# Kernel optimization log

Hardware: AMD Instinct MI355X
Metric: run time of the kernel (lower is better)

Reference implementation:

```python
import jax, jax.numpy as jnp
import numpy as np

V, E, H, L, B, T = 32000, 1024, 1024, 2, 64, 512


def setup_inputs() -> dict:
    key = jax.random.key(0)
    ks = jax.random.split(key, 20)
    s = 0.02  # init scale for params
    n = jax.random.normal
    return {
        "input_tokens": jax.random.randint(ks[0], (1, B), 0, V),
        "h0": n(ks[1], (L, B, H), jnp.float32),
        "c0": n(ks[2], (L, B, H), jnp.float32),
        "encoder_outputs": n(ks[3], (T, B, H), jnp.float32),
        "emb_table": n(ks[4], (V, E), jnp.float32) * s,
        "attn_W": n(ks[5], (H, 2 * H), jnp.float32) * s,
        "attn_b": jnp.zeros((H,), jnp.float32),
        "attn_v": n(ks[6], (H,), jnp.float32) * s,
        "w_ih0": n(ks[7], (4 * H, 2 * E), jnp.float32) * s,
        "w_hh0": n(ks[8], (4 * H, H), jnp.float32) * s,
        "b_ih0": jnp.zeros((4 * H,), jnp.float32),
        "b_hh0": jnp.zeros((4 * H,), jnp.float32),
        "w_ih1": n(ks[9], (4 * H, H), jnp.float32) * s,
        "w_hh1": n(ks[10], (4 * H, H), jnp.float32) * s,
        "b_ih1": jnp.zeros((4 * H,), jnp.float32),
        "b_hh1": jnp.zeros((4 * H,), jnp.float32),
        "out_W": n(ks[11], (V, H), jnp.float32) * s,
        "out_b": jnp.zeros((V,), jnp.float32),
    }


def lstm_cell(x, h, c, w_ih, w_hh, b_ih, b_hh):
    # torch LSTM gate order: i, f, g, o
    g = x @ w_ih.T + h @ w_hh.T + b_ih + b_hh
    i, f, gg, o = jnp.split(g, 4, axis=-1)
    c2 = jax.nn.sigmoid(f) * c + jax.nn.sigmoid(i) * jnp.tanh(gg)
    h2 = jax.nn.sigmoid(o) * jnp.tanh(c2)
    return h2, c2


def reference(input_tokens, h0, c0, encoder_outputs, emb_table, attn_W, attn_b,
              attn_v, w_ih0, w_hh0, b_ih0, b_hh0, w_ih1, w_hh1, b_ih1, b_hh1,
              out_W, out_b):
    emb = emb_table[input_tokens]            # [1, B, E]
    h_top = h0[-1]                           # [B, H]
    # concat attention: score[b,t] = v . (attn_W @ [h_b ; e_tb] + attn_b)
    cat = jnp.concatenate(
        [jnp.broadcast_to(h_top[None], encoder_outputs.shape), encoder_outputs],
        axis=-1)                              # [T, B, 2H]
    scores = jnp.einsum('tbk,hk,h->bt', cat, attn_W, attn_v) \
        + jnp.dot(attn_b, attn_v)            # [B, T]
    attn = jax.nn.softmax(scores, axis=1)    # [B, T]
    context = jnp.einsum('bt,tbh->bh', attn, encoder_outputs)  # [B, H]
    x = jnp.concatenate([context, emb[0]], axis=-1)            # [B, 2E]
    h1, c1 = lstm_cell(x, h0[0], c0[0], w_ih0, w_hh0, b_ih0, b_hh0)
    h2, c2 = lstm_cell(h1, h0[1], c0[1], w_ih1, w_hh1, b_ih1, b_hh1)
    logits = h2 @ out_W.T + out_b            # [B, V]
    out = jax.nn.log_softmax(logits, axis=1)
    h_n = jnp.stack([h1, h2])
    c_n = jnp.stack([c1, c2])
    return out, h_n, c_n, attn[:, None, :]
```

## Files before the change

kernel.cpp:

```cpp
#include <hip/hip_runtime.h>

#define V 32000
#define B 64
#define T 512
#define H 1024

typedef short bf16x8 __attribute__((ext_vector_type(8)));
typedef float f32x4 __attribute__((ext_vector_type(4)));

__device__ inline unsigned short f2bf(float x) {
    unsigned int u = __float_as_uint(x);
    return (unsigned short)((u + 0x7FFFu + ((u >> 16) & 1u)) >> 16);
}

__global__ void prep_misc(const int* __restrict__ tok, const float* __restrict__ emb,
                          const float* __restrict__ h0, unsigned short* __restrict__ xcat0,
                          unsigned short* __restrict__ xcat1, const float4* __restrict__ W4,
                          const float* __restrict__ v, float4* __restrict__ u2p) {
    int blk = blockIdx.x;
    int tid = threadIdx.x;
    if (blk < 256) {
        int idx = blk * 256 + tid;
        int b = idx >> 10, e = idx & 1023;
        xcat0[(size_t)b * 3072 + 1024 + e] = f2bf(emb[(size_t)tok[b] * 1024 + e]);
    } else if (blk < 768) {
        int idx = (blk - 256) * 256 + tid;
        int layer = idx >> 16;
        int r = idx & 65535;
        int b = r >> 10, k = r & 1023;
        float vv = h0[layer * 65536 + b * 1024 + k];
        if (layer == 0) xcat0[(size_t)b * 3072 + 2048 + k] = f2bf(vv);
        else            xcat1[(size_t)b * 2048 + 1024 + k] = f2bf(vv);
    } else {
        int hc = blk - 768;
        float4 acc = {0.f, 0.f, 0.f, 0.f};
#pragma unroll 4
        for (int i = 0; i < 32; ++i) {
            int h = hc * 32 + i;
            float vv = v[h];
            float4 w = W4[(size_t)h * 512 + 256 + tid];
            acc.x += vv * w.x; acc.y += vv * w.y; acc.z += vv * w.z; acc.w += vv * w.w;
        }
        u2p[hc * 256 + tid] = acc;
    }
}

__global__ void u2_reduce(const float4* __restrict__ u2p, float4* __restrict__ u2) {
    int k4 = threadIdx.x;
    float4 acc = {0.f, 0.f, 0.f, 0.f};
#pragma unroll
    for (int hc = 0; hc < 32; ++hc) {
        float4 p = u2p[hc * 256 + k4];
        acc.x += p.x; acc.y += p.y; acc.z += p.z; acc.w += p.w;
    }
    u2[k4] = acc;
}

__global__ __launch_bounds__(256) void attn_fused(
    const float4* __restrict__ enc4, const float4* __restrict__ u2,
    float* __restrict__ scores, float2* __restrict__ pms, float4* __restrict__ ctxp) {
    int b = blockIdx.x;
    int tc = blockIdx.y;
    int tid = threadIdx.x;
    int wid = tid >> 6, lane = tid & 63;
    float4 u[4];
#pragma unroll
    for (int i = 0; i < 4; ++i) u[i] = u2[lane + 64 * i];
    float m = -1e30f, s = 0.f;
    float4 acc[4] = {{0,0,0,0},{0,0,0,0},{0,0,0,0},{0,0,0,0}};
    int t0 = tc * 32 + wid * 8;
    for (int tt = 0; tt < 8; ++tt) {
        int t = t0 + tt;
        const float4* e = enc4 + ((size_t)t * B + b) * 256;
        float4 e4[4];
#pragma unroll
        for (int i = 0; i < 4; ++i) e4[i] = e[lane + 64 * i];
        float d = 0.f;
#pragma unroll
        for (int i = 0; i < 4; ++i)
            d += e4[i].x * u[i].x + e4[i].y * u[i].y + e4[i].z * u[i].z + e4[i].w * u[i].w;
#pragma unroll
        for (int off = 32; off; off >>= 1) d += __shfl_xor(d, off);
        if (lane == 0) scores[b * T + t] = d;
        float mn = fmaxf(m, d);
        float sc = expf(m - mn);
        float w = expf(d - mn);
        s = s * sc + w;
#pragma unroll
        for (int i = 0; i < 4; ++i) {
            acc[i].x = acc[i].x * sc + w * e4[i].x;
            acc[i].y = acc[i].y * sc + w * e4[i].y;
            acc[i].z = acc[i].z * sc + w * e4[i].z;
            acc[i].w = acc[i].w * sc + w * e4[i].w;
        }
        m = mn;
    }
    __shared__ float4 lacc[4][256];
    __shared__ float lm[4], ls[4];
#pragma unroll
    for (int i = 0; i < 4; ++i) lacc[wid][lane + 64 * i] = acc[i];
    if (lane == 0) { lm[wid] = m; ls[wid] = s; }
    __syncthreads();
    float M = fmaxf(fmaxf(lm[0], lm[1]), fmaxf(lm[2], lm[3]));
    float e0 = expf(lm[0] - M), e1 = expf(lm[1] - M);
    float e2 = expf(lm[2] - M), e3 = expf(lm[3] - M);
    float S = ls[0] * e0 + ls[1] * e1 + ls[2] * e2 + ls[3] * e3;
    float4 c0 = lacc[0][tid], c1 = lacc[1][tid], c2 = lacc[2][tid], c3 = lacc[3][tid];
    float4 c;
    c.x = c0.x * e0 + c1.x * e1 + c2.x * e2 + c3.x * e3;
    c.y = c0.y * e0 + c1.y * e1 + c2.y * e2 + c3.y * e3;
    c.z = c0.z * e0 + c1.z * e1 + c2.z * e2 + c3.z * e3;
    c.w = c0.w * e0 + c1.w * e1 + c2.w * e2 + c3.w * e3;
    ctxp[((size_t)tc * B + b) * 256 + tid] = c;
    if (tid == 0) pms[tc * B + b] = make_float2(M, S);
}

__global__ void attn_combine(const float4* __restrict__ ctxp, const float2* __restrict__ pms,
                             const float* __restrict__ scores, unsigned short* __restrict__ xcat0,
                             float* __restrict__ attn_out) {
    int b = blockIdx.x, tid = threadIdx.x;
    float M = -1e30f, S = 0.f;
#pragma unroll
    for (int tc = 0; tc < 16; ++tc) {
        float2 p = pms[tc * B + b];
        float mn = fmaxf(M, p.x);
        S = S * expf(M - mn) + p.y * expf(p.x - mn);
        M = mn;
    }
    float inv = 1.f / S;
    float4 c = {0.f, 0.f, 0.f, 0.f};
#pragma unroll
    for (int tc = 0; tc < 16; ++tc) {
        float w = expf(pms[tc * B + b].x - M);
        float4 v = ctxp[((size_t)tc * B + b) * 256 + tid];
        c.x += w * v.x; c.y += w * v.y; c.z += w * v.z; c.w += w * v.w;
    }
    c.x *= inv; c.y *= inv; c.z *= inv; c.w *= inv;
    unsigned short* d = xcat0 + (size_t)b * 3072 + tid * 4;
    d[0] = f2bf(c.x); d[1] = f2bf(c.y); d[2] = f2bf(c.z); d[3] = f2bf(c.w);
#pragma unroll
    for (int j = 0; j < 2; ++j) {
        int t = j * 256 + tid;
        attn_out[b * T + t] = expf(scores[b * T + t] - M) * inv;
    }
}

struct MJob {
    const float* W1; int ldw1;
    const float* W2; int ldw2;
    int seg;
    const unsigned short* A; int lda;
    float* out; int ldo; long outz;
    const float* bias;
    int kblk;
};

template <int NT>
__global__ __launch_bounds__(256) void mfma_gemm(MJob job) {
    constexpr int CHB = NT * 512;
    __shared__ __align__(16) char Wlds[2 * CHB];
    int tid = threadIdx.x;
    int l = tid & 63;
    int mt = __builtin_amdgcn_readfirstlane(tid >> 6);
    int l15 = l & 15, l4 = l >> 4;
    int n0 = blockIdx.x * NT;
    int kbase = blockIdx.z * job.kblk;
    float* outp = job.out + (size_t)blockIdx.z * job.outz;
    f32x4 acc[NT / 16];
#pragma unroll
    for (int i = 0; i < NT / 16; ++i) acc[i] = (f32x4){0.f, 0.f, 0.f, 0.f};
    int nch = job.kblk >> 7;

    auto stageW = [&](int kg, int bi) {
        const float* Wb; int ldw, koff;
        if (kg < job.seg) { Wb = job.W1; ldw = job.ldw1; koff = kg; }
        else              { Wb = job.W2; ldw = job.ldw2; koff = kg - job.seg; }
        char* base = &Wlds[bi * CHB];
#pragma unroll
        for (int i = 0; i < NT / 8; ++i) {
            int gl = i * 256 + tid;
            int row = gl >> 5, gp = gl & 31;
            int G = gp ^ (row & 7);
            const float* src = Wb + (size_t)(n0 + row) * ldw + koff + G * 4;
            char* dst = base + (i * 4096 + (tid & 192) * 16);
            __builtin_amdgcn_global_load_lds(
                (const __attribute__((address_space(1))) void*)src,
                (__attribute__((address_space(3))) void*)dst, 16, 0, 0);
        }
    };

    stageW(kbase, 0);
    __syncthreads();
    int cur = 0;
    for (int c = 0; c < nch; ++c) {
        int kg = kbase + c * 128;
        bf16x8 af[4];
        const unsigned short* arow = job.A + (size_t)(mt * 16 + l15) * job.lda + kg + l4 * 8;
#pragma unroll
        for (int s = 0; s < 4; ++s) af[s] = *(const bf16x8*)(arow + s * 32);
        if (c + 1 < nch) stageW(kbase + (c + 1) * 128, cur ^ 1);
        const char* rb = &Wlds[cur * CHB];
#pragma unroll
        for (int jt = 0; jt < NT / 16; ++jt) {
            int row = jt * 16 + l15;
            const char* rbase = rb + row * 512;
            int x = row & 7;
#pragma unroll
            for (int s = 0; s < 4; ++s) {
                int G0 = 2 * l4 + 8 * s;
                uint4 wa = *(const uint4*)(rbase + ((G0 ^ x) << 4));
                uint4 wb = *(const uint4*)(rbase + (((G0 + 1) ^ x) << 4));
                union { bf16x8 f; unsigned int u[4]; } bu;
                bu.u[0] = __builtin_amdgcn_perm(wa.y, wa.x, 0x07060302u);
                bu.u[1] = __builtin_amdgcn_perm(wa.w, wa.z, 0x07060302u);
                bu.u[2] = __builtin_amdgcn_perm(wb.y, wb.x, 0x07060302u);
                bu.u[3] = __builtin_amdgcn_perm(wb.w, wb.z, 0x07060302u);
                acc[jt] = __builtin_amdgcn_mfma_f32_16x16x32_bf16(af[s], bu.f, acc[jt], 0, 0, 0);
            }
        }
        __syncthreads();
        cur ^= 1;
    }
#pragma unroll
    for (int jt = 0; jt < NT / 16; ++jt) {
        int n = n0 + jt * 16 + l15;
        float bv = job.bias ? job.bias[n] : 0.f;
#pragma unroll
        for (int r = 0; r < 4; ++r) {
            int m = mt * 16 + l4 * 4 + r;
            outp[(size_t)m * job.ldo + n] = acc[jt][r] + bv;
        }
    }
}

__global__ void lstm_elem(const float* __restrict__ gp, int gz,
                          const float* __restrict__ b_ih, const float* __restrict__ b_hh,
                          const float* __restrict__ c_prev, float* __restrict__ h_out,
                          float* __restrict__ c_out, unsigned short* __restrict__ hbf,
                          int hbf_ld) {
    int idx = blockIdx.x * 256 + threadIdx.x;
    int b = idx >> 10, k = idx & 1023;
    float g[4];
#pragma unroll
    for (int gt = 0; gt < 4; ++gt) {
        float s = b_ih[gt * 1024 + k] + b_hh[gt * 1024 + k];
        for (int z = 0; z < gz; ++z)
            s += gp[(size_t)z * 262144 + (size_t)b * 4096 + gt * 1024 + k];
        g[gt] = s;
    }
    float i_ = 1.f / (1.f + expf(-g[0]));
    float f_ = 1.f / (1.f + expf(-g[1]));
    float gg = tanhf(g[2]);
    float o_ = 1.f / (1.f + expf(-g[3]));
    float c = f_ * c_prev[b * 1024 + k] + i_ * gg;
    float h = o_ * tanhf(c);
    c_out[b * 1024 + k] = c;
    h_out[b * 1024 + k] = h;
    hbf[(size_t)b * hbf_ld + k] = f2bf(h);
}

__global__ void lse_partial(const float4* __restrict__ logits4, float* __restrict__ pm,
                            float* __restrict__ ps) {
    int bi = blockIdx.x;
    int b = bi >> 4, c = bi & 15;
    int tid = threadIdx.x;
    const float4* row = logits4 + (size_t)b * 8000 + c * 500;
    float m = -1e30f, s = 0.f;
#pragma unroll
    for (int i = 0; i < 2; ++i) {
        int v = i * 256 + tid;
        if (v < 500) {
            float4 x = row[v];
            float m1 = fmaxf(fmaxf(x.x, x.y), fmaxf(x.z, x.w));
            if (m1 > m) { s = s * expf(m - m1); m = m1; }
            s += expf(x.x - m) + expf(x.y - m) + expf(x.z - m) + expf(x.w - m);
        }
    }
#pragma unroll
    for (int off = 32; off; off >>= 1) {
        float m2 = __shfl_xor(m, off);
        float s2 = __shfl_xor(s, off);
        float mn = fmaxf(m, m2);
        s = s * expf(m - mn) + s2 * expf(m2 - mn);
        m = mn;
    }
    __shared__ float mred[4], sred[4];
    int wid = tid >> 6, lane = tid & 63;
    if (lane == 0) { mred[wid] = m; sred[wid] = s; }
    __syncthreads();
    if (tid == 0) {
        float M = mred[0], S = sred[0];
        for (int i = 1; i < 4; ++i) {
            float mn = fmaxf(M, mred[i]);
            S = S * expf(M - mn) + sred[i] * expf(mred[i] - mn);
            M = mn;
        }
        pm[bi] = M;
        ps[bi] = S;
    }
}

__global__ void lse_sub(float4* __restrict__ logits4, const float* __restrict__ pm,
                        const float* __restrict__ ps) {
    int b = blockIdx.y;
    float M = pm[b * 16], S = ps[b * 16];
#pragma unroll
    for (int i = 1; i < 16; ++i) {
        float m2 = pm[b * 16 + i];
        float mn = fmaxf(M, m2);
        S = S * expf(M - mn) + ps[b * 16 + i] * expf(m2 - mn);
        M = mn;
    }
    float l = M + logf(S);
    int v4 = blockIdx.x * 256 + threadIdx.x;
    if (v4 < 8000) {
        float4 x = logits4[(size_t)b * 8000 + v4];
        x.x -= l; x.y -= l; x.z -= l; x.w -= l;
        logits4[(size_t)b * 8000 + v4] = x;
    }
}

extern "C" void kernel_launch(void* const* d_in, const int* in_sizes, int n_in,
                              void* d_out, int out_size, void* d_ws, size_t ws_size,
                              hipStream_t stream) {
    const int*   tok   = (const int*)d_in[0];
    const float* h0    = (const float*)d_in[1];
    const float* c0    = (const float*)d_in[2];
    const float* enc   = (const float*)d_in[3];
    const float* emb   = (const float*)d_in[4];
    const float* attnW = (const float*)d_in[5];
    const float* attnv = (const float*)d_in[7];
    const float* w_ih0 = (const float*)d_in[8];
    const float* w_hh0 = (const float*)d_in[9];
    const float* b_ih0 = (const float*)d_in[10];
    const float* b_hh0 = (const float*)d_in[11];
    const float* w_ih1 = (const float*)d_in[12];
    const float* w_hh1 = (const float*)d_in[13];
    const float* b_ih1 = (const float*)d_in[14];
    const float* b_hh1 = (const float*)d_in[15];
    const float* out_W = (const float*)d_in[16];
    const float* out_b = (const float*)d_in[17];
    float* out = (float*)d_out;
    float* ws = (float*)d_ws;

    float* u2     = ws;
    float* u2p    = ws + 1024;
    float* scores = ws + 33792;
    float2* pms   = (float2*)(ws + 66560);
    unsigned short* xcat0 = (unsigned short*)(ws + 68608);
    unsigned short* xcat1 = (unsigned short*)(ws + 166912);
    unsigned short* h2bf  = (unsigned short*)(ws + 232448);
    float* pm     = ws + 265216;
    float* ps     = ws + 266240;

    float* out_logits = out;
    float* out_h1 = out + 2048000;
    float* out_h2 = out + 2113536;
    float* out_c1 = out + 2179072;
    float* out_c2 = out + 2244608;
    float* out_attn = out + 2310144;

    float* ctxp  = out;
    float* gpart = out;

    prep_misc<<<800, 256, 0, stream>>>(tok, emb, h0, xcat0, xcat1,
                                       (const float4*)attnW, attnv, (float4*)u2p);
    u2_reduce<<<1, 256, 0, stream>>>((const float4*)u2p, (float4*)u2);
    attn_fused<<<dim3(64, 16), 256, 0, stream>>>((const float4*)enc, (const float4*)u2,
                                                 scores, pms, (float4*)ctxp);
    attn_combine<<<64, 256, 0, stream>>>((const float4*)ctxp, pms, scores, xcat0, out_attn);

    {
        MJob j = {w_ih0, 2048, w_hh0, 1024, 2048, xcat0, 3072,
                  gpart, 4096, 262144L, nullptr, 768};
        mfma_gemm<64><<<dim3(64, 1, 4), 256, 0, stream>>>(j);
    }
    lstm_elem<<<256, 256, 0, stream>>>(gpart, 4, b_ih0, b_hh0, c0,
                                       out_h1, out_c1, xcat1, 2048);

    {
        MJob j = {w_ih1, 1024, w_hh1, 1024, 1024, xcat1, 2048,
                  gpart, 4096, 262144L, nullptr, 512};
        mfma_gemm<64><<<dim3(64, 1, 4), 256, 0, stream>>>(j);
    }
    lstm_elem<<<256, 256, 0, stream>>>(gpart, 4, b_ih1, b_hh1, c0 + 65536,
                                       out_h2, out_c2, h2bf, 1024);

    {
        MJob j = {out_W, 1024, nullptr, 0, 1 << 30, h2bf, 1024,
                  out_logits, V, 0L, out_b, 1024};
        mfma_gemm<32><<<dim3(1000, 1, 1), 256, 0, stream>>>(j);
    }

    lse_partial<<<1024, 256, 0, stream>>>((const float4*)out_logits, pm, ps);
    lse_sub<<<dim3(32, 64), 256, 0, stream>>>((float4*)out_logits, pm, ps);
}
```

Baseline: 147.7 us.

## Overlap attention with context-independent LSTM gate GEMM slices in one fused launch

Merges the attention kernel with GEMM blocks that compute the layer-0 embedding/hidden K-slices and the layer-1 hidden-state slice, which do not depend on the attention context. These run concurrently in one launch, so the remaining post-attention GEMMs handle only one K-slice each. It also moves the partial buffers into separate workspace regions and branches the online softmax update to skip one exp. The cost is a heterogeneous kernel whose shared-memory size and register use are set by the larger path, plus more partial-sum traffic.

```diff
diff --git a/kernel.cpp b/kernel.cpp
--- a/kernel.cpp
+++ b/kernel.cpp
@@ -56,63 +56,160 @@
     u2[k4] = acc;
 }
 
-__global__ __launch_bounds__(256) void attn_fused(
+struct GSlice {
+    const float* W1; int ldw1;
+    const float* W2; int ldw2;
+    int seg;
+    const unsigned short* A; int lda;
+    float* out;
+    int kbase;
+};
+
+__global__ __launch_bounds__(256) void mega1(
     const float4* __restrict__ enc4, const float4* __restrict__ u2,
-    float* __restrict__ scores, float2* __restrict__ pms, float4* __restrict__ ctxp) {
-    int b = blockIdx.x;
-    int tc = blockIdx.y;
+    float* __restrict__ scores, float2* __restrict__ pms, float4* __restrict__ ctxp,
+    GSlice s0, GSlice s1, GSlice s2) {
+    __shared__ __align__(16) char smem[32768];
+    int bx = blockIdx.x;
     int tid = threadIdx.x;
     int wid = tid >> 6, lane = tid & 63;
-    float4 u[4];
-#pragma unroll
-    for (int i = 0; i < 4; ++i) u[i] = u2[lane + 64 * i];
-    float m = -1e30f, s = 0.f;
-    float4 acc[4] = {{0,0,0,0},{0,0,0,0},{0,0,0,0},{0,0,0,0}};
-    int t0 = tc * 32 + wid * 8;
-    for (int tt = 0; tt < 8; ++tt) {
-        int t = t0 + tt;
-        const float4* e = enc4 + ((size_t)t * B + b) * 256;
-        float4 e4[4];
-#pragma unroll
-        for (int i = 0; i < 4; ++i) e4[i] = e[lane + 64 * i];
-        float d = 0.f;
-#pragma unroll
-        for (int i = 0; i < 4; ++i)
-            d += e4[i].x * u[i].x + e4[i].y * u[i].y + e4[i].z * u[i].z + e4[i].w * u[i].w;
-#pragma unroll
-        for (int off = 32; off; off >>= 1) d += __shfl_xor(d, off);
-        if (lane == 0) scores[b * T + t] = d;
-        float mn = fmaxf(m, d);
-        float sc = expf(m - mn);
-        float w = expf(d - mn);
-        s = s * sc + w;
+
+    if (bx < 1024) {
+        int b = bx & 63, tc = bx >> 6;
+        float4* lacc = (float4*)smem;
+        float* lm = (float*)(smem + 16384);
+        float* ls = (float*)(smem + 16384 + 16);
+        float4 u[4];
+#pragma unroll
+        for (int i = 0; i < 4; ++i) u[i] = u2[lane + 64 * i];
+        float m = -1e30f, s = 0.f;
+        float4 acc[4] = {{0,0,0,0},{0,0,0,0},{0,0,0,0},{0,0,0,0}};
+        int t0 = tc * 32 + wid * 8;
+        for (int tt = 0; tt < 8; ++tt) {
+            int t = t0 + tt;
+            const float4* e = enc4 + ((size_t)t * B + b) * 256;
+            float4 e4[4];
+#pragma unroll
+            for (int i = 0; i < 4; ++i) e4[i] = e[lane + 64 * i];
+            float d = 0.f;
+#pragma unroll
+            for (int i = 0; i < 4; ++i)
+                d += e4[i].x * u[i].x + e4[i].y * u[i].y + e4[i].z * u[i].z + e4[i].w * u[i].w;
+#pragma unroll
+            for (int off = 32; off; off >>= 1) d += __shfl_xor(d, off);
+            if (lane == 0) scores[b * T + t] = d;
+            if (d > m) {
+                float sc = expf(m - d);
+                s = s * sc + 1.f;
+#pragma unroll
+                for (int i = 0; i < 4; ++i) {
+                    acc[i].x = acc[i].x * sc + e4[i].x;
+                    acc[i].y = acc[i].y * sc + e4[i].y;
+                    acc[i].z = acc[i].z * sc + e4[i].z;
+                    acc[i].w = acc[i].w * sc + e4[i].w;
+                }
+                m = d;
+            } else {
+                float w = expf(d - m);
+                s += w;
+#pragma unroll
+                for (int i = 0; i < 4; ++i) {
+                    acc[i].x += w * e4[i].x;
+                    acc[i].y += w * e4[i].y;
+                    acc[i].z += w * e4[i].z;
+                    acc[i].w += w * e4[i].w;
+                }
+            }
+        }
+#pragma unroll
+        for (int i = 0; i < 4; ++i) lacc[wid * 256 + lane + 64 * i] = acc[i];
+        if (lane == 0) { lm[wid] = m; ls[wid] = s; }
+        __syncthreads();
+        float M = fmaxf(fmaxf(lm[0], lm[1]), fmaxf(lm[2], lm[3]));
+        float e0 = expf(lm[0] - M), e1 = expf(lm[1] - M);
+        float e2 = expf(lm[2] - M), e3 = expf(lm[3] - M);
+        float S = ls[0] * e0 + ls[1] * e1 + ls[2] * e2 + ls[3] * e3;
+        float4 c0 = lacc[0 * 256 + tid], c1 = lacc[1 * 256 + tid];
+        float4 c2 = lacc[2 * 256 + tid], c3 = lacc[3 * 256 + tid];
+        float4 c;
+        c.x = c0.x * e0 + c1.x * e1 + c2.x * e2 + c3.x * e3;
+        c.y = c0.y * e0 + c1.y * e1 + c2.y * e2 + c3.y * e3;
+        c.z = c0.z * e0 + c1.z * e1 + c2.z * e2 + c3.z * e3;
+        c.w = c0.w * e0 + c1.w * e1 + c2.w * e2 + c3.w * e3;
+        ctxp[((size_t)tc * B + b) * 256 + tid] = c;
+        if (tid == 0) pms[tc * B + b] = make_float2(M, S);
+        return;
+    }
+
+    int idx = bx - 1024;
+    GSlice g = (idx < 128) ? s0 : (idx < 256) ? s1 : s2;
+    int nb = idx & 127;
+    int l15 = lane & 15, l4 = lane >> 4;
+    int mt = __builtin_amdgcn_readfirstlane(wid);
+    int n0 = nb * 32;
+    f32x4 acc[2];
+    acc[0] = (f32x4){0.f, 0.f, 0.f, 0.f};
+    acc[1] = (f32x4){0.f, 0.f, 0.f, 0.f};
+
+    auto stageW = [&](int kg, int bi) {
+        const float* Wb; int ldw, koff;
+        if (kg < g.seg) { Wb = g.W1; ldw = g.ldw1; koff = kg; }
+        else            { Wb = g.W2; ldw = g.ldw2; koff = kg - g.seg; }
+        char* base = &smem[bi * 16384];
 #pragma unroll
         for (int i = 0; i < 4; ++i) {
-            acc[i].x = acc[i].x * sc + w * e4[i].x;
-            acc[i].y = acc[i].y * sc + w * e4[i].y;
-            acc[i].z = acc[i].z * sc + w * e4[i].z;
-            acc[i].w = acc[i].w * sc + w * e4[i].w;
-        }
-        m = mn;
-    }
-    __shared__ float4 lacc[4][256];
-    __shared__ float lm[4], ls[4];
-#pragma unroll
-    for (int i = 0; i < 4; ++i) lacc[wid][lane + 64 * i] = acc[i];
-    if (lane == 0) { lm[wid] = m; ls[wid] = s; }
+            int gl = i * 256 + tid;
+            int row = gl >> 5, gp = gl & 31;
+            int G = gp ^ (row & 7);
+            const float* src = Wb + (size_t)(n0 + row) * ldw + koff + G * 4;
+            char* dst = base + (i * 4096 + (tid & 192) * 16);
+            __builtin_amdgcn_global_load_lds(
+                (const __attribute__((address_space(1))) void*)src,
+                (__attribute__((address_space(3))) void*)dst, 16, 0, 0);
+        }
+    };
+
+    stageW(g.kbase, 0);
     __syncthreads();
-    float M = fmaxf(fmaxf(lm[0], lm[1]), fmaxf(lm[2], lm[3]));
-    float e0 = expf(lm[0] - M), e1 = expf(lm[1] - M);
-    float e2 = expf(lm[2] - M), e3 = expf(lm[3] - M);
-    float S = ls[0] * e0 + ls[1] * e1 + ls[2] * e2 + ls[3] * e3;
-    float4 c0 = lacc[0][tid], c1 = lacc[1][tid], c2 = lacc[2][tid], c3 = lacc[3][tid];
-    float4 c;
-    c.x = c0.x * e0 + c1.x * e1 + c2.x * e2 + c3.x * e3;
-    c.y = c0.y * e0 + c1.y * e1 + c2.y * e2 + c3.y * e3;
-    c.z = c0.z * e0 + c1.z * e1 + c2.z * e2 + c3.z * e3;
-    c.w = c0.w * e0 + c1.w * e1 + c2.w * e2 + c3.w * e3;
-    ctxp[((size_t)tc * B + b) * 256 + tid] = c;
-    if (tid == 0) pms[tc * B + b] = make_float2(M, S);
+    int cur = 0;
+    for (int c = 0; c < 8; ++c) {
+        int kg = g.kbase + c * 128;
+        bf16x8 af[4];
+        const unsigned short* arow = g.A + (size_t)(mt * 16 + l15) * g.lda + kg + l4 * 8;
+#pragma unroll
+        for (int s = 0; s < 4; ++s) af[s] = *(const bf16x8*)(arow + s * 32);
+        if (c + 1 < 8) stageW(g.kbase + (c + 1) * 128, cur ^ 1);
+        const char* rb = &smem[cur * 16384];
+#pragma unroll
+        for (int jt = 0; jt < 2; ++jt) {
+            int row = jt * 16 + l15;
+            const char* rbase = rb + row * 512;
+            int x = row & 7;
+#pragma unroll
+            for (int s = 0; s < 4; ++s) {
+                int G0 = 2 * l4 + 8 * s;
+                uint4 wa = *(const uint4*)(rbase + ((G0 ^ x) << 4));
+                uint4 wb = *(const uint4*)(rbase + (((G0 + 1) ^ x) << 4));
+                union { bf16x8 f; unsigned int u[4]; } bu;
+                bu.u[0] = __builtin_amdgcn_perm(wa.y, wa.x, 0x07060302u);
+                bu.u[1] = __builtin_amdgcn_perm(wa.w, wa.z, 0x07060302u);
+                bu.u[2] = __builtin_amdgcn_perm(wb.y, wb.x, 0x07060302u);
+                bu.u[3] = __builtin_amdgcn_perm(wb.w, wb.z, 0x07060302u);
+                acc[jt] = __builtin_amdgcn_mfma_f32_16x16x32_bf16(af[s], bu.f, acc[jt], 0, 0, 0);
+            }
+        }
+        __syncthreads();
+        cur ^= 1;
+    }
+#pragma unroll
+    for (int jt = 0; jt < 2; ++jt) {
+        int n = n0 + jt * 16 + l15;
+#pragma unroll
+        for (int r = 0; r < 4; ++r) {
+            int m2 = mt * 16 + l4 * 4 + r;
+            g.out[(size_t)m2 * 4096 + n] = acc[jt][r];
+        }
+    }
 }
 
 __global__ void attn_combine(const float4* __restrict__ ctxp, const float2* __restrict__ pms,
@@ -352,6 +449,9 @@
     unsigned short* h2bf  = (unsigned short*)(ws + 232448);
     float* pm     = ws + 265216;
     float* ps     = ws + 266240;
+    float* ctxp   = ws + 524288;
+    float* gpartL0 = ws + 1572864;
+    float* gpartL1 = ws + 2359296;
 
     float* out_logits = out;
     float* out_h1 = out + 2048000;
@@ -360,30 +460,33 @@
     float* out_c2 = out + 2244608;
     float* out_attn = out + 2310144;
 
-    float* ctxp  = out;
-    float* gpart = out;
-
     prep_misc<<<800, 256, 0, stream>>>(tok, emb, h0, xcat0, xcat1,
                                        (const float4*)attnW, attnv, (float4*)u2p);
     u2_reduce<<<1, 256, 0, stream>>>((const float4*)u2p, (float4*)u2);
-    attn_fused<<<dim3(64, 16), 256, 0, stream>>>((const float4*)enc, (const float4*)u2,
-                                                 scores, pms, (float4*)ctxp);
+
+    {
+        GSlice a = {w_ih0, 2048, w_hh0, 1024, 2048, xcat0, 3072, gpartL0 + 262144,  1024};
+        GSlice b2 = {w_ih0, 2048, w_hh0, 1024, 2048, xcat0, 3072, gpartL0 + 524288, 2048};
+        GSlice c2 = {w_ih1, 1024, w_hh1, 1024, 1024, xcat1, 2048, gpartL1 + 262144, 1024};
+        mega1<<<1408, 256, 0, stream>>>((const float4*)enc, (const float4*)u2,
+                                        scores, pms, (float4*)ctxp, a, b2, c2);
+    }
     attn_combine<<<64, 256, 0, stream>>>((const float4*)ctxp, pms, scores, xcat0, out_attn);
 
     {
         MJob j = {w_ih0, 2048, w_hh0, 1024, 2048, xcat0, 3072,
-                  gpart, 4096, 262144L, nullptr, 768};
-        mfma_gemm<64><<<dim3(64, 1, 4), 256, 0, stream>>>(j);
-    }
-    lstm_elem<<<256, 256, 0, stream>>>(gpart, 4, b_ih0, b_hh0, c0,
+                  gpartL0, 4096, 0L, nullptr, 1024};
+        mfma_gemm<64><<<dim3(64, 1, 1), 256, 0, stream>>>(j);
+    }
+    lstm_elem<<<256, 256, 0, stream>>>(gpartL0, 3, b_ih0, b_hh0, c0,
                                        out_h1, out_c1, xcat1, 2048);
 
     {
         MJob j = {w_ih1, 1024, w_hh1, 1024, 1024, xcat1, 2048,
-                  gpart, 4096, 262144L, nullptr, 512};
-        mfma_gemm<64><<<dim3(64, 1, 4), 256, 0, stream>>>(j);
-    }
-    lstm_elem<<<256, 256, 0, stream>>>(gpart, 4, b_ih1, b_hh1, c0 + 65536,
+                  gpartL1, 4096, 0L, nullptr, 1024};
+        mfma_gemm<64><<<dim3(64, 1, 1), 256, 0, stream>>>(j);
+    }
+    lstm_elem<<<256, 256, 0, stream>>>(gpartL1, 2, b_ih1, b_hh1, c0 + 65536,
                                        out_h2, out_c2, h2bf, 1024);
 
     {
```

Result: slower. 167.8 us (+13.6%).

## Split attention kernel into score pass and weighted-sum pass over encoder chunk

Applied to the files above, without the earlier changes.

Replaces the per-warp online-softmax accumulation with a two-phase scheme: first compute all 32 scores of the chunk into shared memory, then compute chunk max/sum once and have every thread re-read the encoder rows to accumulate the weighted context. This removes the per-step rescaling, the large shared-memory cross-warp merge, and register pressure from holding encoder vectors. The cost is a second read of the encoder chunk (likely from L2), which doubles encoder traffic for this kernel.

```diff
diff --git a/kernel.cpp b/kernel.cpp
--- a/kernel.cpp
+++ b/kernel.cpp
@@ -63,56 +63,48 @@
     int tc = blockIdx.y;
     int tid = threadIdx.x;
     int wid = tid >> 6, lane = tid & 63;
+    __shared__ float sd[32];
+    __shared__ float sw[32];
     float4 u[4];
 #pragma unroll
     for (int i = 0; i < 4; ++i) u[i] = u2[lane + 64 * i];
-    float m = -1e30f, s = 0.f;
-    float4 acc[4] = {{0,0,0,0},{0,0,0,0},{0,0,0,0},{0,0,0,0}};
     int t0 = tc * 32 + wid * 8;
+#pragma unroll
     for (int tt = 0; tt < 8; ++tt) {
         int t = t0 + tt;
         const float4* e = enc4 + ((size_t)t * B + b) * 256;
-        float4 e4[4];
-#pragma unroll
-        for (int i = 0; i < 4; ++i) e4[i] = e[lane + 64 * i];
         float d = 0.f;
 #pragma unroll
-        for (int i = 0; i < 4; ++i)
-            d += e4[i].x * u[i].x + e4[i].y * u[i].y + e4[i].z * u[i].z + e4[i].w * u[i].w;
+        for (int i = 0; i < 4; ++i) {
+            float4 e4 = e[lane + 64 * i];
+            d += e4.x * u[i].x + e4.y * u[i].y + e4.z * u[i].z + e4.w * u[i].w;
+        }
 #pragma unroll
         for (int off = 32; off; off >>= 1) d += __shfl_xor(d, off);
-        if (lane == 0) scores[b * T + t] = d;
-        float mn = fmaxf(m, d);
-        float sc = expf(m - mn);
-        float w = expf(d - mn);
-        s = s * sc + w;
-#pragma unroll
-        for (int i = 0; i < 4; ++i) {
-            acc[i].x = acc[i].x * sc + w * e4[i].x;
-            acc[i].y = acc[i].y * sc + w * e4[i].y;
-            acc[i].z = acc[i].z * sc + w * e4[i].z;
-            acc[i].w = acc[i].w * sc + w * e4[i].w;
-        }
-        m = mn;
-    }
-    __shared__ float4 lacc[4][256];
-    __shared__ float lm[4], ls[4];
-#pragma unroll
-    for (int i = 0; i < 4; ++i) lacc[wid][lane + 64 * i] = acc[i];
-    if (lane == 0) { lm[wid] = m; ls[wid] = s; }
+        if (lane == 0) sd[wid * 8 + tt] = d;
+    }
     __syncthreads();
-    float M = fmaxf(fmaxf(lm[0], lm[1]), fmaxf(lm[2], lm[3]));
-    float e0 = expf(lm[0] - M), e1 = expf(lm[1] - M);
-    float e2 = expf(lm[2] - M), e3 = expf(lm[3] - M);
-    float S = ls[0] * e0 + ls[1] * e1 + ls[2] * e2 + ls[3] * e3;
-    float4 c0 = lacc[0][tid], c1 = lacc[1][tid], c2 = lacc[2][tid], c3 = lacc[3][tid];
-    float4 c;
-    c.x = c0.x * e0 + c1.x * e1 + c2.x * e2 + c3.x * e3;
-    c.y = c0.y * e0 + c1.y * e1 + c2.y * e2 + c3.y * e3;
-    c.z = c0.z * e0 + c1.z * e1 + c2.z * e2 + c3.z * e3;
-    c.w = c0.w * e0 + c1.w * e1 + c2.w * e2 + c3.w * e3;
-    ctxp[((size_t)tc * B + b) * 256 + tid] = c;
+    float M = -1e30f;
+#pragma unroll
+    for (int i = 0; i < 32; ++i) M = fmaxf(M, sd[i]);
+    float S = 0.f;
+#pragma unroll
+    for (int i = 0; i < 32; ++i) S += expf(sd[i] - M);
+    if (tid < 32) {
+        float d = sd[tid];
+        sw[tid] = expf(d - M);
+        scores[b * T + tc * 32 + tid] = d;
+    }
     if (tid == 0) pms[tc * B + b] = make_float2(M, S);
+    __syncthreads();
+    float4 acc = {0.f, 0.f, 0.f, 0.f};
+#pragma unroll 4
+    for (int t = 0; t < 32; ++t) {
+        float w = sw[t];
+        float4 e4 = enc4[((size_t)(tc * 32 + t) * B + b) * 256 + tid];
+        acc.x += w * e4.x; acc.y += w * e4.y; acc.z += w * e4.z; acc.w += w * e4.w;
+    }
+    ctxp[((size_t)tc * B + b) * 256 + tid] = acc;
 }
 
 __global__ void attn_combine(const float4* __restrict__ ctxp, const float2* __restrict__ pms,
```

After: 160.5 us. +8.6%, slower.
